# Optimization experiments

Hardware: AMD Instinct MI355X
Metric: run time of the kernel (lower is better)

The kernel has to match this reference:

```python
import jax, jax.numpy as jnp
import numpy as np

T = 5
EPS = 1e-05
G = 4      # num_groups
D = 64     # num_channels per group


def setup_inputs() -> dict:
    key = jax.random.key(0)
    X = jax.random.normal(key, (32, 256, 56, 56), dtype=jnp.float32)
    weight = jnp.ones((1, 256, 1, 1), dtype=jnp.float32)
    bias = jnp.zeros((1, 256, 1, 1), dtype=jnp.float32)
    return {"X": X, "weight": weight, "bias": bias}


def reference(X, weight, bias):
    N, C, H, W = X.shape
    # (N,C,H,W) -> (C,N,H,W) -> (g, d, m) with m = N*H*W
    x = X.transpose(1, 0, 2, 3).reshape(G, D, -1)
    m = x.shape[-1]
    mean = x.mean(-1, keepdims=True)                 # (g, d, 1)
    xc = x - mean
    I = jnp.eye(D, dtype=X.dtype)
    # Sigma = eps*I + xc xc^T / m     (g, d, d)
    Sigma = EPS * I + jnp.einsum('gdm,gem->gde', xc, xc) / m
    # trace normalization
    rTr = 1.0 / jnp.trace(Sigma, axis1=1, axis2=2)[:, None, None]  # (g,1,1)
    Sn = Sigma * rTr
    # Newton-Schulz iterations: P_{k+1} = 1.5 P_k - 0.5 P_k^3 Sn
    P = jnp.broadcast_to(I, (G, D, D))
    for _ in range(T):
        P = 1.5 * P - 0.5 * (P @ P @ P @ Sn)
    wm = P * jnp.sqrt(rTr)                           # whitening matrix (g,d,d)
    xn = wm @ xc                                     # (g, d, m)
    Xh = xn.reshape(C, N, H, W).transpose(1, 0, 2, 3)
    return Xh * weight + bias
```

## Files before the change

### kernel.cpp

```cpp
#include <hip/hip_runtime.h>
#include <math.h>

#define GROUPS 4
#define DCH    64
#define NBATCH 32
#define CTOT   256
#define HW     3136
#define CHW    (CTOT*HW)
#define MTOT   (NBATCH*HW)
#define PB     196
#define EPSV   1e-5f

typedef __attribute__((ext_vector_type(8))) short bf16x8;
typedef __attribute__((ext_vector_type(4))) float f32x4;

__device__ __forceinline__ f32x4 mfma16(bf16x8 a, bf16x8 b, f32x4 c) {
    return __builtin_amdgcn_mfma_f32_16x16x32_bf16(a, b, c, 0, 0, 0);
}

__device__ __forceinline__ void split2(float x, short& h, short& l) {
    union { float f; unsigned u; } c; c.f = x;
    h = (short)(c.u >> 16);
    union { unsigned u; float f; } hm; hm.u = c.u & 0xFFFF0000u;
    union { float f; unsigned u; } lo; lo.f = x - hm.f;
    l = (short)(lo.u >> 16);
}

__device__ __forceinline__ void load_slab(const float* bp, float dst[16]) {
    float4 a0 = *reinterpret_cast<const float4*>(bp);
    float4 a1 = *reinterpret_cast<const float4*>(bp + 4);
    float4 b0 = *reinterpret_cast<const float4*>(bp + 32);
    float4 b1 = *reinterpret_cast<const float4*>(bp + 36);
    dst[0]=a0.x; dst[1]=a0.y; dst[2]=a0.z;  dst[3]=a0.w;
    dst[4]=a1.x; dst[5]=a1.y; dst[6]=a1.z;  dst[7]=a1.w;
    dst[8]=b0.x; dst[9]=b0.y; dst[10]=b0.z; dst[11]=b0.w;
    dst[12]=b1.x; dst[13]=b1.y; dst[14]=b1.z; dst[15]=b1.w;
}

__global__ __launch_bounds__(512) void k1_gram(const float* __restrict__ X,
                                               float* __restrict__ pGram,
                                               float* __restrict__ pSum)
{
    constexpr int KPB = MTOT / PB;
    constexpr int NST = KPB / 128;
    const int pb   = blockIdx.x;
    const int g    = blockIdx.y;
    const int tid  = threadIdx.x;
    const int w    = tid >> 6;
    const int lane = tid & 63;
    const int tr   = w & 3;
    const int par  = w >> 2;
    const int lr   = lane & 15;
    const int q    = lane >> 4;

    __shared__ float smem[8192];
    __shared__ float rsum[2][64];

    f32x4 acc[4];
#pragma unroll
    for (int c = 0; c < 4; ++c) acc[c] = (f32x4)(0.f);
    float sumv = 0.f;

    const float* Xg  = X + (size_t)g * DCH * HW;
    const int    row = 16 * tr + lr;

    float xv[2][16];
    {
        const int kk = pb * KPB + par * 64;
        const int n  = kk / HW;
        const int s  = kk - n * HW;
        load_slab(Xg + (size_t)n * CHW + (size_t)row * HW + s + q * 8, xv[0]);
    }

#pragma unroll
    for (int t = 0; t < NST; ++t) {
        if (t + 1 < NST) {
            const int kk = pb * KPB + (t + 1) * 128 + par * 64;
            const int n  = kk / HW;
            const int s  = kk - n * HW;
            load_slab(Xg + (size_t)n * CHW + (size_t)row * HW + s + q * 8,
                      xv[(t + 1) & 1]);
        }
        bf16x8 ah[2], al[2];
#pragma unroll
        for (int ks = 0; ks < 2; ++ks) {
#pragma unroll
            for (int j = 0; j < 8; ++j) {
                float x = xv[t & 1][ks * 8 + j];
                sumv += x;
                short h, l; split2(x, h, l);
                ah[ks][j] = h; al[ks][j] = l;
            }
        }
#pragma unroll
        for (int ks = 0; ks < 2; ++ks) {
            *reinterpret_cast<bf16x8*>(&smem[(((par*4+tr)*2+ks)*2+0)*256 + lane*4]) = ah[ks];
            *reinterpret_cast<bf16x8*>(&smem[(((par*4+tr)*2+ks)*2+1)*256 + lane*4]) = al[ks];
        }
        __syncthreads();
#pragma unroll
        for (int c = 0; c < 4; ++c) {
#pragma unroll
            for (int ks = 0; ks < 2; ++ks) {
                bf16x8 bh = *reinterpret_cast<const bf16x8*>(
                    &smem[(((par*4+c)*2+ks)*2+0)*256 + lane*4]);
                bf16x8 bl = *reinterpret_cast<const bf16x8*>(
                    &smem[(((par*4+c)*2+ks)*2+1)*256 + lane*4]);
                acc[c] = mfma16(ah[ks], bh, acc[c]);
                acc[c] = mfma16(ah[ks], bl, acc[c]);
                acc[c] = mfma16(al[ks], bh, acc[c]);
            }
        }
        __syncthreads();
    }

    sumv += __shfl_xor(sumv, 16);
    sumv += __shfl_xor(sumv, 32);
    if (q == 0) rsum[par][row] = sumv;

#pragma unroll
    for (int c = 0; c < 4; ++c) {
#pragma unroll
        for (int r = 0; r < 4; ++r) {
            smem[par * 4096 + (16 * tr + 4 * q + r) * 64 + 16 * c + lr] = acc[c][r];
        }
    }
    __syncthreads();

    float* pg = pGram + ((size_t)g * PB + pb) * 4096;
    for (int i = tid; i < 4096; i += 512) pg[i] = smem[i] + smem[4096 + i];
    if (tid < 64)
        pSum[((size_t)g * PB + pb) * 64 + tid] = rsum[0][tid] + rsum[1][tid];
}

__global__ __launch_bounds__(256) void k2a1(const float* __restrict__ pGram,
                                            const float* __restrict__ pSum,
                                            float* __restrict__ pG2,
                                            float* __restrict__ pS2)
{
    constexpr int SLICE = PB / 7;
    const int cb  = blockIdx.x;
    const int g   = blockIdx.y;
    const int s   = blockIdx.z;
    const int tid = threadIdx.x;
    const int e = tid & 63, q = tid >> 6;
    __shared__ float red[4][64];
    __shared__ float red2[4][64];

    const float* pg = pGram + ((size_t)g * PB + s * SLICE + q) * 4096 + cb * 64 + e;
    float sum = 0.f;
#pragma unroll
    for (int i = 0; i < SLICE / 4; ++i)
        sum += pg[(size_t)i * 4 * 4096];
    red[q][e] = sum;
    if (cb == 0) {
        const float* ps = pSum + ((size_t)g * PB + s * SLICE + q) * 64 + e;
        float s2 = 0.f;
#pragma unroll
        for (int i = 0; i < SLICE / 4; ++i)
            s2 += ps[i * 4 * 64];
        red2[q][e] = s2;
    }
    __syncthreads();
    if (tid < 64) {
        pG2[((size_t)g * 7 + s) * 4096 + cb * 64 + tid] =
            red[0][tid] + red[1][tid] + red[2][tid] + red[3][tid];
        if (cb == 0)
            pS2[((size_t)g * 7 + s) * 64 + tid] =
                red2[0][tid] + red2[1][tid] + red2[2][tid] + red2[3][tid];
    }
}

__device__ __forceinline__ void packrow2(const float* __restrict__ M, int row, int q,
                                         bf16x8& h0, bf16x8& l0,
                                         bf16x8& h1, bf16x8& l1)
{
    const float* p = M + row * 68 + 8 * q;
    float4 a0 = *reinterpret_cast<const float4*>(p);
    float4 a1 = *reinterpret_cast<const float4*>(p + 4);
    float4 b0 = *reinterpret_cast<const float4*>(p + 32);
    float4 b1 = *reinterpret_cast<const float4*>(p + 36);
    float e0[8] = {a0.x, a0.y, a0.z, a0.w, a1.x, a1.y, a1.z, a1.w};
    float e1[8] = {b0.x, b0.y, b0.z, b0.w, b1.x, b1.y, b1.z, b1.w};
#pragma unroll
    for (int j = 0; j < 8; ++j) {
        short h, l;
        split2(e0[j], h, l); h0[j] = h; l0[j] = l;
        split2(e1[j], h, l); h1[j] = h; l1[j] = l;
    }
}

__global__ __launch_bounds__(256) void k2b_ns(const float* __restrict__ pG2,
                                              const float* __restrict__ pS2,
                                              const float* __restrict__ Wt,
                                              const float* __restrict__ Bs,
                                              float* __restrict__ Aout,
                                              float* __restrict__ Off)
{
    const int g   = blockIdx.x;
    const int tid = threadIdx.x;
    const int w = tid >> 6, lane = tid & 63, lr = lane & 15, q = lane >> 4;
    __shared__ float MP[64 * 68];
    __shared__ float MA[64 * 68];
    __shared__ float MB2[64 * 68];
    __shared__ float MS[64 * 68];
    __shared__ float lmean[64];
    __shared__ float redm[1024];
    __shared__ float rtr_s;

    if (tid < 64) {
        float s2 = 0.f;
#pragma unroll
        for (int s = 0; s < 7; ++s) s2 += pS2[((size_t)g * 7 + s) * 64 + tid];
        lmean[tid] = s2 * (1.0f / (float)MTOT);
    }
    __syncthreads();
    for (int idx = tid; idx < 4096; idx += 256) {
        int d = idx >> 6, e = idx & 63;
        float sum = 0.f;
#pragma unroll
        for (int s = 0; s < 7; ++s) sum += pG2[((size_t)g * 7 + s) * 4096 + idx];
        float v = sum * (1.0f / (float)MTOT) - lmean[d] * lmean[e];
        if (d == e) v += EPSV;
        MS[d * 68 + e] = v;
    }
    __syncthreads();
    if (tid < 64) {
        float v = MS[tid * 68 + tid];
#pragma unroll
        for (int off = 32; off > 0; off >>= 1) v += __shfl_down(v, off);
        if (tid == 0) rtr_s = 1.f / v;
    }
    __syncthreads();
    const float rTr = rtr_s;
    for (int idx = tid; idx < 4096; idx += 256) {
        int d = idx >> 6, e = idx & 63;
        float sv = MS[d * 68 + e] * rTr;
        MS[d * 68 + e] = sv;
        MP[d * 68 + e] = ((d == e) ? 1.5f : 0.f) - 0.5f * sv;
    }
    __syncthreads();

    const int row_o = 16 * w + 4 * q;
    for (int it = 0; it < 4; ++it) {
        f32x4 a2[4], aS[4];
#pragma unroll
        for (int c = 0; c < 4; ++c) { a2[c] = (f32x4)(0.f); aS[c] = (f32x4)(0.f); }
        bf16x8 pah0, pal0, pah1, pal1;
        packrow2(MP, 16 * w + lr, q, pah0, pal0, pah1, pal1);
#pragma unroll
        for (int c = 0; c < 4; ++c) {
            bf16x8 bh0, bl0, bh1, bl1;
            packrow2(MP, 16 * c + lr, q, bh0, bl0, bh1, bl1);
            a2[c] = mfma16(pah0, bh0, a2[c]);
            a2[c] = mfma16(pah0, bl0, a2[c]);
            a2[c] = mfma16(pal0, bh0, a2[c]);
            a2[c] = mfma16(pah1, bh1, a2[c]);
            a2[c] = mfma16(pah1, bl1, a2[c]);
            a2[c] = mfma16(pal1, bh1, a2[c]);
            bf16x8 sh0, sl0, sh1, sl1;
            packrow2(MS, 16 * c + lr, q, sh0, sl0, sh1, sl1);
            aS[c] = mfma16(pah0, sh0, aS[c]);
            aS[c] = mfma16(pah0, sl0, aS[c]);
            aS[c] = mfma16(pal0, sh0, aS[c]);
            aS[c] = mfma16(pah1, sh1, aS[c]);
            aS[c] = mfma16(pah1, sl1, aS[c]);
            aS[c] = mfma16(pal1, sh1, aS[c]);
        }
#pragma unroll
        for (int c = 0; c < 4; ++c)
#pragma unroll
            for (int r = 0; r < 4; ++r) {
                MA [(row_o + r) * 68 + 16 * c + lr] = a2[c][r];
                MB2[(row_o + r) * 68 + 16 * c + lr] = aS[c][r];
            }
        __syncthreads();

        f32x4 acc[4];
#pragma unroll
        for (int c = 0; c < 4; ++c) acc[c] = (f32x4)(0.f);
        bf16x8 qah0, qal0, qah1, qal1;
        packrow2(MA, 16 * w + lr, q, qah0, qal0, qah1, qal1);
#pragma unroll
        for (int c = 0; c < 4; ++c) {
            bf16x8 bh0, bl0, bh1, bl1;
            packrow2(MB2, 16 * c + lr, q, bh0, bl0, bh1, bl1);
            acc[c] = mfma16(qah0, bh0, acc[c]);
            acc[c] = mfma16(qah0, bl0, acc[c]);
            acc[c] = mfma16(qal0, bh0, acc[c]);
            acc[c] = mfma16(qah1, bh1, acc[c]);
            acc[c] = mfma16(qah1, bl1, acc[c]);
            acc[c] = mfma16(qal1, bh1, acc[c]);
        }
#pragma unroll
        for (int c = 0; c < 4; ++c)
#pragma unroll
            for (int r = 0; r < 4; ++r) {
                int o = (row_o + r) * 68 + 16 * c + lr;
                MP[o] = 1.5f * MP[o] - 0.5f * acc[c][r];
            }
        __syncthreads();
    }

    const float sc = sqrtf(rTr);
    const int i0 = (tid >> 4) << 2, j0 = (tid & 15) << 2;
#pragma unroll
    for (int i = 0; i < 4; ++i) {
        int d = i0 + i;
        float wv = Wt[g * 64 + d] * sc;
        float4 v;
        v.x = MP[d * 68 + j0 + 0] * wv;
        v.y = MP[d * 68 + j0 + 1] * wv;
        v.z = MP[d * 68 + j0 + 2] * wv;
        v.w = MP[d * 68 + j0 + 3] * wv;
        *reinterpret_cast<float4*>(Aout + g * 4096 + (d << 6) + j0) = v;
        redm[(d << 4) + (tid & 15)] =
            v.x * lmean[j0] + v.y * lmean[j0 + 1] + v.z * lmean[j0 + 2] + v.w * lmean[j0 + 3];
    }
    __syncthreads();
    if (tid < 64) {
        float s = 0.f;
#pragma unroll
        for (int qq = 0; qq < 16; ++qq) s += redm[(tid << 4) + qq];
        Off[g * 64 + tid] = Bs[g * 64 + tid] - s;
    }
}

__global__ __launch_bounds__(256) void k3_apply(const float* __restrict__ X,
                                                const float* __restrict__ Aout,
                                                const float* __restrict__ Off,
                                                float* __restrict__ Y)
{
    const int c    = blockIdx.x;
    const int g    = blockIdx.y;
    const int tid  = threadIdx.x;
    const int w    = tid >> 6;
    const int lane = tid & 63;
    const int lr   = lane & 15;
    const int q    = lane >> 4;

    __shared__ float tile[4096];

    const int col0 = c * 64;
    const int n    = col0 / HW;
    const int s0   = col0 - n * HW;
    const float* Xg   = X + (size_t)g * DCH * HW;
    const float* base = Xg + (size_t)n * CHW + s0;

    float4 xr[4];
#pragma unroll
    for (int k = 0; k < 4; ++k) {
        int f = k * 256 + tid, r = f >> 4, gc = f & 15;
        xr[k] = *reinterpret_cast<const float4*>(base + (size_t)r * HW + gc * 4);
    }

    bf16x8 ah[2], al[2];
#pragma unroll
    for (int s = 0; s < 2; ++s) {
        const float* ap = Aout + g * 4096 + (16 * w + lr) * 64 + 32 * s + 8 * q;
        float4 v0 = *reinterpret_cast<const float4*>(ap);
        float4 v1 = *reinterpret_cast<const float4*>(ap + 4);
        float av[8] = {v0.x, v0.y, v0.z, v0.w, v1.x, v1.y, v1.z, v1.w};
#pragma unroll
        for (int j = 0; j < 8; ++j) {
            short h, l; split2(av[j], h, l);
            ah[s][j] = h; al[s][j] = l;
        }
    }
    float offv[4];
#pragma unroll
    for (int r = 0; r < 4; ++r) offv[r] = Off[g * 64 + 16 * w + 4 * q + r];

#pragma unroll
    for (int k = 0; k < 4; ++k) {
        int f = k * 256 + tid;
        *reinterpret_cast<float4*>(&tile[f * 4]) = xr[k];
    }
    __syncthreads();

    f32x4 accg[4];
#pragma unroll
    for (int j = 0; j < 4; ++j) accg[j] = (f32x4)(0.f);

#pragma unroll
    for (int ks = 0; ks < 2; ++ks) {
        bf16x8 bh[4], bl[4];
#pragma unroll
        for (int j8 = 0; j8 < 8; ++j8) {
            const int row = 32 * ks + 8 * q + j8;
            float4 v = *reinterpret_cast<const float4*>(&tile[row * 64 + lr * 4]);
            float vv[4] = {v.x, v.y, v.z, v.w};
#pragma unroll
            for (int jj = 0; jj < 4; ++jj) {
                short h, l; split2(vv[jj], h, l);
                bh[jj][j8] = h; bl[jj][j8] = l;
            }
        }
#pragma unroll
        for (int jj = 0; jj < 4; ++jj) {
            accg[jj] = mfma16(ah[ks], bh[jj], accg[jj]);
            accg[jj] = mfma16(ah[ks], bl[jj], accg[jj]);
            accg[jj] = mfma16(al[ks], bh[jj], accg[jj]);
        }
    }

    float* yp = Y + (size_t)g * DCH * HW + (size_t)n * CHW + s0 + 4 * lr;
#pragma unroll
    for (int r = 0; r < 4; ++r) {
        int row = 16 * w + 4 * q + r;
        float4 o;
        o.x = accg[0][r] + offv[r];
        o.y = accg[1][r] + offv[r];
        o.z = accg[2][r] + offv[r];
        o.w = accg[3][r] + offv[r];
        *reinterpret_cast<float4*>(yp + (size_t)row * HW) = o;
    }
}

extern "C" void kernel_launch(void* const* d_in, const int* in_sizes, int n_in,
                              void* d_out, int out_size, void* d_ws, size_t ws_size,
                              hipStream_t stream)
{
    const float* X  = (const float*)d_in[0];
    const float* Wt = (const float*)d_in[1];
    const float* Bs = (const float*)d_in[2];
    float* Y  = (float*)d_out;
    float* ws = (float*)d_ws;

    float* pGram = ws;
    float* pSum  = pGram + (size_t)4 * PB * 4096;
    float* pG2   = pSum  + (size_t)4 * PB * 64;
    float* pS2   = pG2   + (size_t)4 * 7 * 4096;
    float* Aout  = pS2   + (size_t)4 * 7 * 64;
    float* Off   = Aout  + 4 * 4096;

    k1_gram <<<dim3(PB, GROUPS), 512, 0, stream>>>(X, pGram, pSum);
    k2a1    <<<dim3(64, GROUPS, 7), 256, 0, stream>>>(pGram, pSum, pG2, pS2);
    k2b_ns  <<<dim3(GROUPS), 256, 0, stream>>>(pG2, pS2, Wt, Bs, Aout, Off);
    k3_apply<<<dim3(1568, GROUPS), 256, 0, stream>>>(X, Aout, Off, Y);
}
```

Before: 81.84 us.

## Deepen stats prefetch, hoist Sn packing, load apply tile directly to registers

The covariance pass now keeps three register buffers in flight (prefetch distance two) and uses a sched_barrier so loads are issued before the conversion work. The Newton-Schulz loop packs the constant Sn matrix into bf16 hi/lo fragments once instead of on every iteration. The apply kernel drops its shared-memory staging tile and __syncthreads, so each wave loads the exact float4s it needs straight from global memory into registers. This costs more VGPRs, which may lower occupancy, and in the apply kernel the four waves now each fetch the same 64x64 input tile instead of sharing one copy through LDS.

Result: slower. 83.80 us (+2.4%).

```diff
diff --git a/kernel.cpp b/kernel.cpp
--- a/kernel.cpp
+++ b/kernel.cpp
@@ -64,29 +64,31 @@
     const float* Xg  = X + (size_t)g * DCH * HW;
     const int    row = 16 * tr + lr;
 
-    float xv[2][16];
-    {
-        const int kk = pb * KPB + par * 64;
+    float xv[3][16];
+#pragma unroll
+    for (int t0 = 0; t0 < 2; ++t0) {
+        const int kk = pb * KPB + t0 * 128 + par * 64;
         const int n  = kk / HW;
         const int s  = kk - n * HW;
-        load_slab(Xg + (size_t)n * CHW + (size_t)row * HW + s + q * 8, xv[0]);
+        load_slab(Xg + (size_t)n * CHW + (size_t)row * HW + s + q * 8, xv[t0]);
     }
 
 #pragma unroll
     for (int t = 0; t < NST; ++t) {
-        if (t + 1 < NST) {
-            const int kk = pb * KPB + (t + 1) * 128 + par * 64;
+        if (t + 2 < NST) {
+            const int kk = pb * KPB + (t + 2) * 128 + par * 64;
             const int n  = kk / HW;
             const int s  = kk - n * HW;
             load_slab(Xg + (size_t)n * CHW + (size_t)row * HW + s + q * 8,
-                      xv[(t + 1) & 1]);
-        }
+                      xv[(t + 2) % 3]);
+        }
+        __builtin_amdgcn_sched_barrier(0);
         bf16x8 ah[2], al[2];
 #pragma unroll
         for (int ks = 0; ks < 2; ++ks) {
 #pragma unroll
             for (int j = 0; j < 8; ++j) {
-                float x = xv[t & 1][ks * 8 + j];
+                float x = xv[t % 3][ks * 8 + j];
                 sumv += x;
                 short h, l; split2(x, h, l);
                 ah[ks][j] = h; al[ks][j] = l;
@@ -241,6 +243,11 @@
     }
     __syncthreads();
 
+    bf16x8 snh0[4], snl0[4], snh1[4], snl1[4];
+#pragma unroll
+    for (int c = 0; c < 4; ++c)
+        packrow2(MS, 16 * c + lr, q, snh0[c], snl0[c], snh1[c], snl1[c]);
+
     const int row_o = 16 * w + 4 * q;
     for (int it = 0; it < 4; ++it) {
         f32x4 a2[4], aS[4];
@@ -258,14 +265,12 @@
             a2[c] = mfma16(pah1, bh1, a2[c]);
             a2[c] = mfma16(pah1, bl1, a2[c]);
             a2[c] = mfma16(pal1, bh1, a2[c]);
-            bf16x8 sh0, sl0, sh1, sl1;
-            packrow2(MS, 16 * c + lr, q, sh0, sl0, sh1, sl1);
-            aS[c] = mfma16(pah0, sh0, aS[c]);
-            aS[c] = mfma16(pah0, sl0, aS[c]);
-            aS[c] = mfma16(pal0, sh0, aS[c]);
-            aS[c] = mfma16(pah1, sh1, aS[c]);
-            aS[c] = mfma16(pah1, sl1, aS[c]);
-            aS[c] = mfma16(pal1, sh1, aS[c]);
+            aS[c] = mfma16(pah0, snh0[c], aS[c]);
+            aS[c] = mfma16(pah0, snl0[c], aS[c]);
+            aS[c] = mfma16(pal0, snh0[c], aS[c]);
+            aS[c] = mfma16(pah1, snh1[c], aS[c]);
+            aS[c] = mfma16(pah1, snl1[c], aS[c]);
+            aS[c] = mfma16(pal1, snh1[c], aS[c]);
         }
 #pragma unroll
         for (int c = 0; c < 4; ++c)
@@ -339,20 +344,19 @@
     const int lr   = lane & 15;
     const int q    = lane >> 4;
 
-    __shared__ float tile[4096];
-
     const int col0 = c * 64;
     const int n    = col0 / HW;
     const int s0   = col0 - n * HW;
     const float* Xg   = X + (size_t)g * DCH * HW;
-    const float* base = Xg + (size_t)n * CHW + s0;
-
-    float4 xr[4];
-#pragma unroll
-    for (int k = 0; k < 4; ++k) {
-        int f = k * 256 + tid, r = f >> 4, gc = f & 15;
-        xr[k] = *reinterpret_cast<const float4*>(base + (size_t)r * HW + gc * 4);
-    }
+    const float* base = Xg + (size_t)n * CHW + s0 + 4 * lr;
+
+    float4 xv[16];
+#pragma unroll
+    for (int ks = 0; ks < 2; ++ks)
+#pragma unroll
+        for (int j8 = 0; j8 < 8; ++j8)
+            xv[ks * 8 + j8] =
+                *reinterpret_cast<const float4*>(base + (size_t)(32 * ks + 8 * q + j8) * HW);
 
     bf16x8 ah[2], al[2];
 #pragma unroll
@@ -370,13 +374,7 @@
     float offv[4];
 #pragma unroll
     for (int r = 0; r < 4; ++r) offv[r] = Off[g * 64 + 16 * w + 4 * q + r];
-
-#pragma unroll
-    for (int k = 0; k < 4; ++k) {
-        int f = k * 256 + tid;
-        *reinterpret_cast<float4*>(&tile[f * 4]) = xr[k];
-    }
-    __syncthreads();
+    __builtin_amdgcn_sched_barrier(0);
 
     f32x4 accg[4];
 #pragma unroll
@@ -387,8 +385,7 @@
         bf16x8 bh[4], bl[4];
 #pragma unroll
         for (int j8 = 0; j8 < 8; ++j8) {
-            const int row = 32 * ks + 8 * q + j8;
-            float4 v = *reinterpret_cast<const float4*>(&tile[row * 64 + lr * 4]);
+            float4 v = xv[ks * 8 + j8];
             float vv[4] = {v.x, v.y, v.z, v.w};
 #pragma unroll
             for (int jj = 0; jj < 4; ++jj) {
```
